# Kernel tuning notes

Measured on AMD Instinct MI355X. Metric: run time of the kernel, lower is better.

Reference implementation:

```python
import jax, jax.numpy as jnp
import numpy as np

B, S, HID = 2, 2048, 2048
H, HKV, HD = 16, 8, 128
INPUT_CHUNK, RET_CHUNK = 256, 64
NUM_CHUNKS = S // INPUT_CHUNK - 1          # 7 retrieval chunks
INPUT_START = NUM_CHUNKS * RET_CHUNK       # 448
KV_LEN = S + INPUT_START                   # 2496
SCALE = HD ** -0.5


def _document_id():
    d = np.zeros(KV_LEN, np.int32)
    d[INPUT_START:] = -1
    for i in range(NUM_CHUNKS):            # retrieval chunks get ids 1..NUM_CHUNKS
        d[RET_CHUNK * i: RET_CHUNK * (i + 1)] = i + 1
    for i in range(1, NUM_CHUNKS + 1):     # input chunk i (i>=1) gets id i
        d[INPUT_START + INPUT_CHUNK * i: INPUT_START + INPUT_CHUNK * (i + 1)] = i
    return d


def _causal_retrieval_mask():
    d = _document_id()
    q = np.arange(S)[:, None]
    kv = np.arange(KV_LEN)[None, :]
    causal = (q + INPUT_START >= kv) & (kv > INPUT_START)
    docm = (d[q + INPUT_START] == d[kv]) & (kv < INPUT_START)
    return jnp.asarray(causal | docm)      # [S, KV_LEN] bool


_MASK = _causal_retrieval_mask()


def rotate_half(x):
    x1, x2 = jnp.split(x, 2, axis=-1)
    return jnp.concatenate([-x2, x1], axis=-1)


def setup_inputs() -> dict:
    key = jax.random.key(0)
    ks = jax.random.split(key, 8)
    hidden_states = jax.random.normal(ks[0], (B, S, HID), jnp.float32)
    # standard llama RoPE tables
    pos = jnp.arange(S, dtype=jnp.float32)
    inv = 1.0 / (10000.0 ** (jnp.arange(0, HD, 2, dtype=jnp.float32) / HD))
    f = pos[:, None] * inv[None, :]
    emb = jnp.concatenate([f, f], axis=-1)
    cos = jnp.broadcast_to(jnp.cos(emb), (B, S, HD)).astype(jnp.float32)
    sin = jnp.broadcast_to(jnp.sin(emb), (B, S, HD)).astype(jnp.float32)
    retrieval_key_states = jax.random.normal(ks[1], (B * NUM_CHUNKS, HKV, RET_CHUNK, HD), jnp.float32)
    retrieval_value_states = jax.random.normal(ks[2], (B * NUM_CHUNKS, HKV, RET_CHUNK, HD), jnp.float32)
    s = 0.02
    Wq = jax.random.normal(ks[3], (HID, H * HD), jnp.float32) * s
    Wk = jax.random.normal(ks[4], (HID, HKV * HD), jnp.float32) * s
    Wv = jax.random.normal(ks[5], (HID, HKV * HD), jnp.float32) * s
    Wo = jax.random.normal(ks[6], (H * HD, HID), jnp.float32) * s
    return {"hidden_states": hidden_states, "cos": cos, "sin": sin,
            "retrieval_key_states": retrieval_key_states,
            "retrieval_value_states": retrieval_value_states,
            "Wq": Wq, "Wk": Wk, "Wv": Wv, "Wo": Wo}


def reference(hidden_states, cos, sin, retrieval_key_states, retrieval_value_states, Wq, Wk, Wv, Wo):
    b = hidden_states.shape[0]
    # QKV projections (bias=False), -> [b, h, s, d]
    q = (hidden_states @ Wq).reshape(b, S, H, HD).transpose(0, 2, 1, 3)
    k = (hidden_states @ Wk).reshape(b, S, HKV, HD).transpose(0, 2, 1, 3)
    v = (hidden_states @ Wv).reshape(b, S, HKV, HD).transpose(0, 2, 1, 3)
    # RoPE (cos/sin unsqueezed over heads)
    c = cos[:, None]
    sn = sin[:, None]
    q = q * c + rotate_half(q) * sn
    k = k * c + rotate_half(k) * sn
    # retrieval KV: (b*nc, hkv, rc, d) -> (b, hkv, nc*rc, d)
    rk = retrieval_key_states.reshape(b, NUM_CHUNKS, HKV, RET_CHUNK, HD).transpose(0, 2, 1, 3, 4).reshape(b, HKV, NUM_CHUNKS * RET_CHUNK, HD)
    rv = retrieval_value_states.reshape(b, NUM_CHUNKS, HKV, RET_CHUNK, HD).transpose(0, 2, 1, 3, 4).reshape(b, HKV, NUM_CHUNKS * RET_CHUNK, HD)
    k_all = jnp.concatenate([rk, k], axis=2)     # [b, hkv, KV_LEN, d]
    v_all = jnp.concatenate([rv, v], axis=2)
    # GQA: repeat kv heads
    g = H // HKV
    k_all = jnp.repeat(k_all, g, axis=1)
    v_all = jnp.repeat(v_all, g, axis=1)
    scores = jnp.einsum('bhqd,bhkd->bhqk', q, k_all) * SCALE
    neg = jnp.finfo(scores.dtype).min
    scores = jnp.where(_MASK[None, None], scores, neg)
    probs = jax.nn.softmax(scores, axis=-1)
    # fully-masked rows (q_idx=0) -> 0 output, matching flex_attention semantics
    probs = jnp.where(_MASK[None, None], probs, 0.0)
    attn = jnp.einsum('bhqk,bhkd->bhqd', probs, v_all)   # [b, H, S, HD]
    # NOTE: source reshapes (b, H, S, HD) directly to (b, S, H*HD) with NO transpose
    attn = attn.reshape(b, S, H * HD)
    return attn @ Wo
```

## Files before the change

### kernel.cpp

```cpp
#include <hip/hip_runtime.h>

#define B_ 2
#define S_ 2048
#define HID_ 2048
#define H_ 16
#define HKV_ 8
#define HD_ 128
#define NCH_ 7
#define RET_ 64
#define IST_ 448
#define KVL_ 2496
#define SCALE_ 0.08838834764831845f
#define SC2_ (0.08838834764831845f * 1.44269504088896340f)

typedef __attribute__((ext_vector_type(8))) short short8;
typedef __attribute__((ext_vector_type(4))) float f32x4;

static __device__ __forceinline__ unsigned short f2bf(float f) {
    unsigned u = __float_as_uint(f);
    unsigned r = (u + 0x7fffu + ((u >> 16) & 1u)) >> 16;
    return (unsigned short)r;
}
static __device__ __forceinline__ float bf2f(unsigned short x) {
    return __uint_as_float(((unsigned)x) << 16);
}

template <int CTRL>
static __device__ __forceinline__ float dppf(float x) {
    return __int_as_float(__builtin_amdgcn_update_dpp(
        0, __float_as_int(x), CTRL, 0xF, 0xF, true));
}
static __device__ __forceinline__ float red16_max(float x) {
    x = fmaxf(x, dppf<0xB1>(x));
    x = fmaxf(x, dppf<0x4E>(x));
    x = fmaxf(x, dppf<0x124>(x));
    x = fmaxf(x, dppf<0x128>(x));
    return x;
}
static __device__ __forceinline__ float red16_sum(float x) {
    x += dppf<0xB1>(x);
    x += dppf<0x4E>(x);
    x += dppf<0x124>(x);
    x += dppf<0x128>(x);
    return x;
}

#define GLL16(gp, lp) __builtin_amdgcn_global_load_lds( \
    (__attribute__((address_space(1))) void*)(void*)(gp), \
    (__attribute__((address_space(3))) void*)(void*)(lp), 16, 0, 0)

__global__ __launch_bounds__(256) void cvt_f32_bf16(const float* __restrict__ x,
                                                    unsigned short* __restrict__ y, int n4) {
    int i = blockIdx.x * 256 + threadIdx.x;
    if (i >= n4) return;
    float4 v = ((const float4*)x)[i];
    ushort4 o;
    o.x = f2bf(v.x); o.y = f2bf(v.y); o.z = f2bf(v.z); o.w = f2bf(v.w);
    ((ushort4*)y)[i] = o;
}

__global__ __launch_bounds__(256) void transpose_cvt(const float* __restrict__ W,
                                                     unsigned short* __restrict__ WT,
                                                     int K, int N) {
    __shared__ float t[32][33];
    const int k0 = blockIdx.x << 5, n0 = blockIdx.y << 5;
    const int tx = threadIdx.x, ty = threadIdx.y;
#pragma unroll
    for (int i = 0; i < 4; i++)
        t[ty + i * 8][tx] = W[(size_t)(k0 + ty + i * 8) * N + n0 + tx];
    __syncthreads();
#pragma unroll
    for (int i = 0; i < 4; i++)
        WT[(size_t)(n0 + ty + i * 8) * K + k0 + tx] = f2bf(t[tx][ty + i * 8]);
}

__global__ __launch_bounds__(512, 2) void gemm256(const unsigned short* __restrict__ A,
                                                  const unsigned short* __restrict__ BT,
                                                  unsigned short* __restrict__ C,
                                                  int M, int N, int K) {
    __shared__ short As[2][16384];
    __shared__ short Bs[2][16384];
    const int tid = threadIdx.x;
    const int wid = tid >> 6, lane = tid & 63;
    const int lq = lane & 15, lk = lane >> 4;
    const int wm = wid >> 2, wn = wid & 3;
    const int bm = blockIdx.x, bn = blockIdx.y;

    const int rowin = tid >> 3;
    const int koff = (((tid & 7) ^ (rowin & 7)) << 3);
    const size_t abase = (size_t)(bm * 256 + rowin) * K;
    const size_t bbase = (size_t)(bn * 256 + rowin) * K;
    const int ldst = wid * 512;

    f32x4 acc[8][4] = {};

    auto stage = [&](int buf, int k0) {
#pragma unroll
        for (int r = 0; r < 4; r++) {
            GLL16(A + abase + (size_t)(r * 64) * K + k0 + koff, &As[buf][r * 4096 + ldst]);
            GLL16(BT + bbase + (size_t)(r * 64) * K + k0 + koff, &Bs[buf][r * 4096 + ldst]);
        }
    };

    const int nk = K >> 6;
    stage(0, 0);
    __syncthreads();
    for (int t = 0; t < nk; t++) {
        const int cur = t & 1;
        if (t + 1 < nk) stage(cur ^ 1, (t + 1) << 6);
        short8 bf[2][4];
#pragma unroll
        for (int j = 0; j < 4; j++)
#pragma unroll
            for (int kk = 0; kk < 2; kk++) {
                const int row = wn * 64 + j * 16 + lq;
                bf[kk][j] = *(const short8*)&Bs[cur][row * 64 +
                                                     (((kk * 4 + lk) ^ (lq & 7)) << 3)];
            }
#pragma unroll
        for (int p = 0; p < 4; p++) {
            short8 af0[2], af1[2];
#pragma unroll
            for (int kk = 0; kk < 2; kk++) {
                const int r0 = wm * 128 + (2 * p) * 16 + lq;
                const int r1 = wm * 128 + (2 * p + 1) * 16 + lq;
                af0[kk] = *(const short8*)&As[cur][r0 * 64 +
                                                   (((kk * 4 + lk) ^ (lq & 7)) << 3)];
                af1[kk] = *(const short8*)&As[cur][r1 * 64 +
                                                   (((kk * 4 + lk) ^ (lq & 7)) << 3)];
            }
            __builtin_amdgcn_s_setprio(1);
#pragma unroll
            for (int j = 0; j < 4; j++)
#pragma unroll
                for (int kk = 0; kk < 2; kk++) {
                    acc[2 * p][j] =
                        __builtin_amdgcn_mfma_f32_16x16x32_bf16(bf[kk][j], af0[kk], acc[2 * p][j], 0, 0, 0);
                    acc[2 * p + 1][j] =
                        __builtin_amdgcn_mfma_f32_16x16x32_bf16(bf[kk][j], af1[kk], acc[2 * p + 1][j], 0, 0, 0);
                }
            __builtin_amdgcn_s_setprio(0);
        }
        __syncthreads();
    }
#pragma unroll
    for (int i = 0; i < 8; i++) {
        const size_t row = (size_t)(bm * 256 + wm * 128 + i * 16 + lq);
#pragma unroll
        for (int j = 0; j < 4; j++) {
            const size_t col = (size_t)(bn * 256 + wn * 64 + j * 16 + lk * 4);
            ushort4 u;
            u.x = f2bf(acc[i][j][0]);
            u.y = f2bf(acc[i][j][1]);
            u.z = f2bf(acc[i][j][2]);
            u.w = f2bf(acc[i][j][3]);
            *(ushort4*)&C[row * N + col] = u;
        }
    }
}

static __device__ __forceinline__ void store_out(unsigned short* p, float v) { *p = f2bf(v); }
static __device__ __forceinline__ void store_out(float* p, float v) { *p = v; }

template <typename OT>
__global__ __launch_bounds__(256) void gemm_bt(const unsigned short* __restrict__ A,
                                               const unsigned short* __restrict__ BT,
                                               OT* __restrict__ C,
                                               int M, int N, int K) {
    __shared__ short As[3][4096];
    __shared__ short Bs[3][4096];
    const int tid = threadIdx.x;
    const int wid = tid >> 6, lane = tid & 63;
    const int lq = lane & 15, lk = lane >> 4;
    const int wr = wid >> 1, wc = wid & 1;
    const int bm = blockIdx.x, bn = blockIdx.y;
    f32x4 acc[4][4] = {};
    const int r0 = tid >> 2, kp0 = (tid & 3) * 8;
    const int c1 = tid + 256;
    const int r1 = c1 >> 2, kp1 = (c1 & 3) * 8;
    const size_t arow0 = (size_t)(bm * 128 + r0) * K;
    const size_t arow1 = (size_t)(bm * 128 + r1) * K;
    const size_t brow0 = (size_t)(bn * 128 + r0) * K;
    const size_t brow1 = (size_t)(bn * 128 + r1) * K;

    auto stage = [&](int buf, int k0) {
        GLL16(A + arow0 + k0 + kp0, &As[buf][wid * 512]);
        GLL16(A + arow1 + k0 + kp1, &As[buf][2048 + wid * 512]);
        GLL16(BT + brow0 + k0 + kp0, &Bs[buf][wid * 512]);
        GLL16(BT + brow1 + k0 + kp1, &Bs[buf][2048 + wid * 512]);
    };

    const int nk = K >> 5;
    stage(0, 0);
    stage(1, 32);
    int cb = 0;
    for (int t = 0; t < nk; t++) {
        if (t + 2 < nk) {
            int nb = cb + 2; if (nb >= 3) nb -= 3;
            stage(nb, (t + 2) << 5);
            asm volatile("s_waitcnt vmcnt(8)" ::: "memory");
        } else if (t + 1 < nk) {
            asm volatile("s_waitcnt vmcnt(4)" ::: "memory");
        } else {
            asm volatile("s_waitcnt vmcnt(0)" ::: "memory");
        }
        __syncthreads();
        short8 af[4], bf[4];
#pragma unroll
        for (int i = 0; i < 4; i++)
            af[i] = *(const short8*)(&As[cb][(wr * 64 + i * 16 + lq) * 32 + lk * 8]);
#pragma unroll
        for (int j = 0; j < 4; j++)
            bf[j] = *(const short8*)(&Bs[cb][(wc * 64 + j * 16 + lq) * 32 + lk * 8]);
#pragma unroll
        for (int i = 0; i < 4; i++)
#pragma unroll
            for (int j = 0; j < 4; j++)
                acc[i][j] = __builtin_amdgcn_mfma_f32_16x16x32_bf16(af[i], bf[j], acc[i][j], 0, 0, 0);
        __syncthreads();
        cb++; if (cb >= 3) cb = 0;
    }
#pragma unroll
    for (int i = 0; i < 4; i++)
#pragma unroll
        for (int j = 0; j < 4; j++)
#pragma unroll
            for (int r = 0; r < 4; r++) {
                size_t row = (size_t)bm * 128 + wr * 64 + i * 16 + lk * 4 + r;
                size_t col = (size_t)bn * 128 + wc * 64 + j * 16 + lq;
                store_out(&C[row * N + col], acc[i][j][r]);
            }
}

__global__ __launch_bounds__(256) void rope_q_kernel(const unsigned short* __restrict__ qkvraw,
                                                     const float* __restrict__ cosb,
                                                     const float* __restrict__ sinb,
                                                     unsigned short* __restrict__ qatt) {
    size_t idx = (size_t)blockIdx.x * 256 + threadIdx.x;
    int d = idx & 63;
    int h = (idx >> 6) & 15;
    size_t bs = idx >> 10;
    size_t base = bs * 4096 + h * 128 + d;
    float x1 = bf2f(qkvraw[base]), x2 = bf2f(qkvraw[base + 64]);
    float c1 = cosb[bs * 128 + d], sn1 = sinb[bs * 128 + d];
    float c2 = cosb[bs * 128 + d + 64], sn2 = sinb[bs * 128 + d + 64];
    int b = (int)(bs >> 11), s = (int)(bs & 2047);
    size_t o = ((size_t)(b * H_ + h) * S_ + s) * HD_ + d;
    qatt[o] = f2bf(x1 * c1 - x2 * sn1);
    qatt[o + 64] = f2bf(x2 * c2 + x1 * sn2);
}

__global__ __launch_bounds__(256) void rope_k_kernel(const unsigned short* __restrict__ qkvraw,
                                                     const float* __restrict__ cosb,
                                                     const float* __restrict__ sinb,
                                                     unsigned short* __restrict__ kall) {
    size_t idx = (size_t)blockIdx.x * 256 + threadIdx.x;
    int d = idx & 63;
    int hk = (idx >> 6) & 7;
    size_t bs = idx >> 9;
    size_t base = bs * 4096 + 2048 + hk * 128 + d;
    float x1 = bf2f(qkvraw[base]), x2 = bf2f(qkvraw[base + 64]);
    float c1 = cosb[bs * 128 + d], sn1 = sinb[bs * 128 + d];
    float c2 = cosb[bs * 128 + d + 64], sn2 = sinb[bs * 128 + d + 64];
    int b = (int)(bs >> 11), s = (int)(bs & 2047);
    size_t o = ((size_t)(b * HKV_ + hk) * KVL_ + IST_ + s) * HD_ + d;
    kall[o] = f2bf(x1 * c1 - x2 * sn1);
    kall[o + 64] = f2bf(x2 * c2 + x1 * sn2);
}

__global__ void scatter_v_kernel(const unsigned short* __restrict__ qkvraw,
                                 unsigned short* __restrict__ vt) {
    __shared__ unsigned short t[32][33];
    const int bh = blockIdx.z;
    const int b = bh >> 3, hk = bh & 7;
    const int d0 = blockIdx.x << 5, s0 = blockIdx.y << 5;
    const int tx = threadIdx.x, ty = threadIdx.y;
#pragma unroll
    for (int i = 0; i < 4; i++)
        t[ty + i * 8][tx] =
            qkvraw[(size_t)(b * S_ + s0 + ty + i * 8) * 4096 + 3072 + hk * 128 + d0 + tx];
    __syncthreads();
#pragma unroll
    for (int i = 0; i < 4; i++)
        vt[((size_t)(b * HKV_ + hk) * HD_ + d0 + ty + i * 8) * KVL_ + IST_ + s0 + tx] = t[tx][ty + i * 8];
}

__global__ __launch_bounds__(256) void scatter_rk_kernel(const float* __restrict__ rk,
                                                         unsigned short* __restrict__ kall) {
    size_t idx = (size_t)blockIdx.x * 256 + threadIdx.x;
    int d = idx & 127;
    int r = (idx >> 7) & 63;
    int hk = (idx >> 13) & 7;
    int bc = (int)(idx >> 16);
    int b = bc / NCH_, ch = bc % NCH_;
    kall[((size_t)(b * HKV_ + hk) * KVL_ + ch * RET_ + r) * HD_ + d] = f2bf(rk[idx]);
}

__global__ void scatter_rv_kernel(const float* __restrict__ rv,
                                  unsigned short* __restrict__ vt) {
    __shared__ float t[32][33];
    const int z = blockIdx.z;
    const int bc = z >> 3, hk = z & 7;
    const int b = bc / NCH_, ch = bc % NCH_;
    const int d0 = blockIdx.x << 5, r0 = blockIdx.y << 5;
    const int tx = threadIdx.x, ty = threadIdx.y;
#pragma unroll
    for (int i = 0; i < 4; i++)
        t[ty + i * 8][tx] = rv[((size_t)(bc * HKV_ + hk) * RET_ + r0 + ty + i * 8) * HD_ + d0 + tx];
    __syncthreads();
#pragma unroll
    for (int i = 0; i < 4; i++)
        vt[((size_t)(b * HKV_ + hk) * HD_ + d0 + ty + i * 8) * KVL_ + ch * RET_ + r0 + tx] =
            f2bf(t[tx][ty + i * 8]);
}

__global__ __launch_bounds__(1024) void attn_kernel(const unsigned short* __restrict__ qatt,
                                                    const unsigned short* __restrict__ kall,
                                                    const unsigned short* __restrict__ vt,
                                                    unsigned short* __restrict__ attnb) {
    __shared__ short Ks[2][8192];
    __shared__ short Vs[2][8192];
    __shared__ short Ps[16][1024];
    const int tid = threadIdx.x;
    const int wid = tid >> 6, lane = tid & 63;
    const int lq = lane & 15, lk = lane >> 4;
    const int pairi = blockIdx.x;
    const int h = blockIdx.y, b = blockIdx.z, hk = h >> 1;
    const unsigned short* kbase = kall + (size_t)(b * HKV_ + hk) * KVL_ * HD_;
    const unsigned short* vbase = vt + (size_t)(b * HKV_ + hk) * HD_ * KVL_;

    const int so = tid * 16;
    const int krow = so >> 8;
    const int koffe = (((tid & 15) ^ (krow & 7)) << 3);
    const int vrow = so >> 7;
    const unsigned short* vrp = vbase + (size_t)vrow * KVL_ + (((tid & 7) ^ (vrow & 7)) << 3);
    short* psw = &Ps[wid][0];

    const int qlo = pairi * 128, qhi = (15 - pairi) * 128;
    const int wgrp = wid >> 3;
    const int qb0 = wgrp ? qhi : qlo;
    const int qbw = qb0 + (wid & 7) * 16;
    const int mydoc = qb0 >> 8;
    const int doc_lo = qlo >> 8;
    const int doc_hi = qhi >> 8;
    const int nr = (doc_lo >= 1 ? 2 : 1);
    const int nt = nr + (qhi + 128) / 64;

    const unsigned short* qptr = qatt + ((size_t)(b * H_ + h) * S_ + qbw + lq) * HD_;
    short8 qf[4];
#pragma unroll
    for (int d = 0; d < 4; d++) qf[d] = *(const short8*)(qptr + d * 32 + lk * 8);
    f32x4 o[8] = {};
    float m[4] = {-1e30f, -1e30f, -1e30f, -1e30f};
    float lsum[4] = {0.f, 0.f, 0.f, 0.f};

    auto kvof = [&](int t) -> int {
        if (t < nr) return (nr == 2 && t == 0) ? RET_ * (doc_lo - 1) : RET_ * (doc_hi - 1);
        return IST_ + (t - nr) * 64;
    };
    auto stage = [&](int buf, int kv0) {
        GLL16(kbase + (size_t)(kv0 + krow) * HD_ + koffe, &Ks[buf][wid * 512]);
        GLL16(vrp + kv0, &Vs[buf][wid * 512]);
    };

    stage(0, kvof(0));
    asm volatile("s_waitcnt vmcnt(0)" ::: "memory");
    __syncthreads();
    int cur = 0;
    for (int t = 0; t < nt; t++) {
        if (t + 1 < nt) stage(cur ^ 1, kvof(t + 1));
        const int kv0 = kvof(t);
        const bool isret = (kv0 < IST_);
        const bool active = isret ? (mydoc >= 1 && kv0 == RET_ * (mydoc - 1))
                                  : (kv0 <= qbw + 15 + IST_);
        if (active) {
            const bool needMask = !isret && !((kv0 != IST_) && (kv0 + 63 <= qbw + IST_));
            const char* kb = (const char*)&Ks[cur][0];
            const char* vb = (const char*)&Vs[cur][0];
            f32x4 sa[4] = {};
            __builtin_amdgcn_s_setprio(1);
#pragma unroll
            for (int d = 0; d < 4; d++) {
#pragma unroll
                for (int j = 0; j < 4; j++) {
                    short8 kf = *(const short8*)(kb + ((j * 16 + lq) * 256 +
                                                       (((d * 4 + lk) ^ (lq & 7)) << 4)));
                    sa[j] = __builtin_amdgcn_mfma_f32_16x16x32_bf16(qf[d], kf, sa[j], 0, 0, 0);
                }
            }
            __builtin_amdgcn_s_setprio(0);

            float mxs[4];
            bool need = false;
#pragma unroll
            for (int r = 0; r < 4; r++) {
                if (needMask) {
                    const int qg = qbw + lk * 4 + r;
#pragma unroll
                    for (int j = 0; j < 4; j++) {
                        int kg = kv0 + j * 16 + lq;
                        bool v = (kg > IST_ && kg <= qg + IST_);
                        if (!v) sa[j][r] = -3e38f;
                    }
                }
                float lm = fmaxf(fmaxf(sa[0][r], sa[1][r]), fmaxf(sa[2][r], sa[3][r]));
                mxs[r] = red16_max(lm) * SC2_;
                need = need || (mxs[r] > m[r] + 8.f);
            }
            if (__any((int)need)) {
#pragma unroll
                for (int r = 0; r < 4; r++) {
                    float mn = fmaxf(m[r], mxs[r]);
                    float al = __builtin_amdgcn_exp2f(m[r] - mn);
                    m[r] = mn;
                    lsum[r] *= al;
#pragma unroll
                    for (int db = 0; db < 8; db++) o[db][r] *= al;
                }
            }
#pragma unroll
            for (int r = 0; r < 4; r++) {
                const int prow = lk * 4 + r;
                float rs = 0.f;
#pragma unroll
                for (int j = 0; j < 4; j++) {
                    float p = __builtin_amdgcn_exp2f(fmaf(sa[j][r], SC2_, -m[r]));
                    rs += p;
                    *(short*)((char*)psw + ((prow * 128 + ((j * 16 + lq) << 1)) ^
                                            ((prow & 7) << 4))) = (short)f2bf(p);
                }
                lsum[r] += red16_sum(rs);
            }
            __builtin_amdgcn_s_setprio(1);
#pragma unroll
            for (int ks = 0; ks < 2; ks++) {
                short8 pa = *(const short8*)((const char*)psw +
                                             (lq * 128 + (((ks * 4 + lk) ^ (lq & 7)) << 4)));
#pragma unroll
                for (int db = 0; db < 8; db++) {
                    short8 vf = *(const short8*)(vb + ((db * 16 + lq) * 128 +
                                                       (((ks * 4 + lk) ^ (lq & 7)) << 4)));
                    o[db] = __builtin_amdgcn_mfma_f32_16x16x32_bf16(pa, vf, o[db], 0, 0, 0);
                }
            }
            __builtin_amdgcn_s_setprio(0);
        }
        if (t + 1 < nt) asm volatile("s_waitcnt vmcnt(0)" ::: "memory");
        __syncthreads();
        cur ^= 1;
    }

    float inv[4];
#pragma unroll
    for (int r = 0; r < 4; r++) inv[r] = lsum[r] > 0.f ? 1.f / lsum[r] : 0.f;
#pragma unroll
    for (int db = 0; db < 8; db++)
#pragma unroll
        for (int r = 0; r < 4; r++) {
            int qg = qbw + lk * 4 + r;
            size_t row = (size_t)b * 2048 + h * 128 + (qg >> 4);
            size_t col = (size_t)(qg & 15) * 128 + db * 16 + lq;
            attnb[row * 2048 + col] = f2bf(o[db][r] * inv[r]);
        }
}

extern "C" void kernel_launch(void* const* d_in, const int* in_sizes, int n_in,
                              void* d_out, int out_size, void* d_ws, size_t ws_size,
                              hipStream_t stream) {
    const float* hidden = (const float*)d_in[0];
    const float* cosb = (const float*)d_in[1];
    const float* sinb = (const float*)d_in[2];
    const float* rk = (const float*)d_in[3];
    const float* rv = (const float*)d_in[4];
    const float* Wq = (const float*)d_in[5];
    const float* Wk = (const float*)d_in[6];
    const float* Wv = (const float*)d_in[7];
    const float* Wo = (const float*)d_in[8];
    float* out = (float*)d_out;

    char* ws = (char*)d_ws;
    unsigned short* hb     = (unsigned short*)(ws + 0);
    unsigned short* wqkvT  = (unsigned short*)(ws + 16777216);
    unsigned short* woT    = (unsigned short*)(ws + 33554432);
    unsigned short* qkvraw = (unsigned short*)(ws + 41943040);
    unsigned short* qatt   = (unsigned short*)(ws + 75497472);
    unsigned short* kallb  = (unsigned short*)(ws + 92274688);
    unsigned short* vtb    = (unsigned short*)(ws + 102498304);
    unsigned short* attnb  = (unsigned short*)(ws + 112721920);

    cvt_f32_bf16<<<8192, 256, 0, stream>>>(hidden, hb, 2097152);
    transpose_cvt<<<dim3(64, 64), dim3(32, 8), 0, stream>>>(Wq, wqkvT, 2048, 2048);
    transpose_cvt<<<dim3(64, 32), dim3(32, 8), 0, stream>>>(Wk, wqkvT + (size_t)2048 * 2048, 2048, 1024);
    transpose_cvt<<<dim3(64, 32), dim3(32, 8), 0, stream>>>(Wv, wqkvT + (size_t)3072 * 2048, 2048, 1024);
    transpose_cvt<<<dim3(64, 64), dim3(32, 8), 0, stream>>>(Wo, woT, 2048, 2048);

    gemm256<<<dim3(16, 16), 512, 0, stream>>>(hb, wqkvT, qkvraw, 4096, 4096, 2048);

    rope_q_kernel<<<16384, 256, 0, stream>>>(qkvraw, cosb, sinb, qatt);
    rope_k_kernel<<<8192, 256, 0, stream>>>(qkvraw, cosb, sinb, kallb);
    scatter_v_kernel<<<dim3(4, 64, 16), dim3(32, 8), 0, stream>>>(qkvraw, vtb);
    scatter_rk_kernel<<<3584, 256, 0, stream>>>(rk, kallb);
    scatter_rv_kernel<<<dim3(4, 2, 112), dim3(32, 8), 0, stream>>>(rv, vtb);

    attn_kernel<<<dim3(8, 16, 2), 1024, 0, stream>>>(qatt, kallb, vtb, attnb);

    gemm_bt<float><<<dim3(32, 16), 256, 0, stream>>>(attnb, woT, out, 4096, 2048, 2048);
}
```

Baseline: 259.0 us.

## Split attention blocks into 512-thread single-query-tile blocks with register-staged KV prefetch

The attention kernel no longer pairs a low and a high query tile in one 1024-thread block. It now launches one 128-query tile per 512-thread block, doubling the grid, with launch bounds targeting several blocks per CU. The double-buffered direct global-to-LDS loads are replaced by a single LDS buffer: the next tile is prefetched into registers and written to LDS after a barrier. This aims to cut LDS use and improve occupancy and scheduling flexibility. In exchange it gives up the causal load-balancing pairing, adds an extra barrier per iteration, and uses more registers for the prefetch.

```diff
diff --git a/kernel.cpp b/kernel.cpp
--- a/kernel.cpp
+++ b/kernel.cpp
@@ -314,37 +314,38 @@
             f2bf(t[tx][ty + i * 8]);
 }
 
-__global__ __launch_bounds__(1024) void attn_kernel(const unsigned short* __restrict__ qatt,
-                                                    const unsigned short* __restrict__ kall,
-                                                    const unsigned short* __restrict__ vt,
-                                                    unsigned short* __restrict__ attnb) {
-    __shared__ short Ks[2][8192];
-    __shared__ short Vs[2][8192];
-    __shared__ short Ps[16][1024];
+__global__ __launch_bounds__(512, 4) void attn_kernel(const unsigned short* __restrict__ qatt,
+                                                      const unsigned short* __restrict__ kall,
+                                                      const unsigned short* __restrict__ vt,
+                                                      unsigned short* __restrict__ attnb) {
+    __shared__ short Ks[8192];
+    __shared__ short Vs[8192];
+    __shared__ short Ps[8][1024];
     const int tid = threadIdx.x;
     const int wid = tid >> 6, lane = tid & 63;
     const int lq = lane & 15, lk = lane >> 4;
-    const int pairi = blockIdx.x;
     const int h = blockIdx.y, b = blockIdx.z, hk = h >> 1;
     const unsigned short* kbase = kall + (size_t)(b * HKV_ + hk) * KVL_ * HD_;
     const unsigned short* vbase = vt + (size_t)(b * HKV_ + hk) * HD_ * KVL_;
 
-    const int so = tid * 16;
-    const int krow = so >> 8;
-    const int koffe = (((tid & 15) ^ (krow & 7)) << 3);
-    const int vrow = so >> 7;
-    const unsigned short* vrp = vbase + (size_t)vrow * KVL_ + (((tid & 7) ^ (vrow & 7)) << 3);
+    int krow[2], kdst[2], vrow[2], vdst[2];
+#pragma unroll
+    for (int p = 0; p < 2; p++) {
+        int o = p * 8192 + tid * 16;
+        int kr = o >> 8;
+        krow[p] = kr;
+        kdst[p] = kr * 128 + (((tid & 15) ^ (kr & 7)) << 3);
+        int vr = o >> 7;
+        vrow[p] = vr;
+        vdst[p] = vr * 64 + (((tid & 7) ^ (vr & 7)) << 3);
+    }
     short* psw = &Ps[wid][0];
 
-    const int qlo = pairi * 128, qhi = (15 - pairi) * 128;
-    const int wgrp = wid >> 3;
-    const int qb0 = wgrp ? qhi : qlo;
-    const int qbw = qb0 + (wid & 7) * 16;
-    const int mydoc = qb0 >> 8;
-    const int doc_lo = qlo >> 8;
-    const int doc_hi = qhi >> 8;
-    const int nr = (doc_lo >= 1 ? 2 : 1);
-    const int nt = nr + (qhi + 128) / 64;
+    const int qb0 = blockIdx.x * 128;
+    const int qbw = qb0 + wid * 16;
+    const int doc = qb0 >> 8;
+    const int nr = (doc >= 1 ? 1 : 0);
+    const int nt = nr + (qb0 + 128) / 64;
 
     const unsigned short* qptr = qatt + ((size_t)(b * H_ + h) * S_ + qbw + lq) * HD_;
     short8 qf[4];
@@ -355,28 +356,37 @@
     float lsum[4] = {0.f, 0.f, 0.f, 0.f};
 
     auto kvof = [&](int t) -> int {
-        if (t < nr) return (nr == 2 && t == 0) ? RET_ * (doc_lo - 1) : RET_ * (doc_hi - 1);
-        return IST_ + (t - nr) * 64;
+        return (t < nr) ? RET_ * (doc - 1) : IST_ + (t - nr) * 64;
     };
-    auto stage = [&](int buf, int kv0) {
-        GLL16(kbase + (size_t)(kv0 + krow) * HD_ + koffe, &Ks[buf][wid * 512]);
-        GLL16(vrp + kv0, &Vs[buf][wid * 512]);
+
+    uint4 kreg[2], vreg[2];
+    auto loadr = [&](int kv0) {
+#pragma unroll
+        for (int p = 0; p < 2; p++) {
+            kreg[p] = *(const uint4*)(kbase + (size_t)(kv0 + krow[p]) * HD_ + (tid & 15) * 8);
+            vreg[p] = *(const uint4*)(vbase + (size_t)vrow[p] * KVL_ + kv0 + (tid & 7) * 8);
+        }
     };
-
-    stage(0, kvof(0));
-    asm volatile("s_waitcnt vmcnt(0)" ::: "memory");
+    auto writelds = [&]() {
+#pragma unroll
+        for (int p = 0; p < 2; p++) {
+            *(uint4*)&Ks[kdst[p]] = kreg[p];
+            *(uint4*)&Vs[vdst[p]] = vreg[p];
+        }
+    };
+
+    loadr(kvof(0));
+    writelds();
     __syncthreads();
-    int cur = 0;
     for (int t = 0; t < nt; t++) {
-        if (t + 1 < nt) stage(cur ^ 1, kvof(t + 1));
+        if (t + 1 < nt) loadr(kvof(t + 1));
         const int kv0 = kvof(t);
         const bool isret = (kv0 < IST_);
-        const bool active = isret ? (mydoc >= 1 && kv0 == RET_ * (mydoc - 1))
-                                  : (kv0 <= qbw + 15 + IST_);
+        const bool active = isret || (kv0 <= qbw + 15 + IST_);
         if (active) {
             const bool needMask = !isret && !((kv0 != IST_) && (kv0 + 63 <= qbw + IST_));
-            const char* kb = (const char*)&Ks[cur][0];
-            const char* vb = (const char*)&Vs[cur][0];
+            const char* kb = (const char*)&Ks[0];
+            const char* vb = (const char*)&Vs[0];
             f32x4 sa[4] = {};
             __builtin_amdgcn_s_setprio(1);
 #pragma unroll
@@ -445,9 +455,11 @@
             }
             __builtin_amdgcn_s_setprio(0);
         }
-        if (t + 1 < nt) asm volatile("s_waitcnt vmcnt(0)" ::: "memory");
         __syncthreads();
-        cur ^= 1;
+        if (t + 1 < nt) {
+            writelds();
+            __syncthreads();
+        }
     }
 
     float inv[4];
@@ -502,7 +514,7 @@
     scatter_rk_kernel<<<3584, 256, 0, stream>>>(rk, kallb);
     scatter_rv_kernel<<<dim3(4, 2, 112), dim3(32, 8), 0, stream>>>(rv, vtb);
 
-    attn_kernel<<<dim3(8, 16, 2), 1024, 0, stream>>>(qatt, kallb, vtb, attnb);
+    attn_kernel<<<dim3(16, 16, 2), 512, 0, stream>>>(qatt, kallb, vtb, attnb);
 
     gemm_bt<float><<<dim3(32, 16), 256, 0, stream>>>(attnb, woT, out, 4096, 2048, 2048);
 }
```

After: 354.5 us. +36.9%, slower.
